# Optimization experiments

Measured on AMD Instinct MI355X. Metric: run time of the kernel, lower is better.

Reference implementation:

```python
import jax, jax.numpy as jnp
import numpy as np

N, E, E_LG, H, KGE, NUM_GRAPHS, N_ITER = 100000, 500000, 1000000, 128, 128, 1024, 2
EPS = 1e-5

def _prelu(x, a):
    return jnp.where(x >= 0, x, a * x)

def _seg_mean(vals, idx, num):
    s = jax.ops.segment_sum(vals, idx, num_segments=num)
    c = jax.ops.segment_sum(jnp.ones((vals.shape[0],), vals.dtype), idx, num_segments=num)
    return s / jnp.maximum(c, 1.0)[:, None]

def setup_inputs() -> dict:
    key = jax.random.key(0)
    ks = jax.random.split(key, 16)
    sc = 1.0 / np.sqrt(H)
    inp = {
        "x": jax.random.normal(ks[0], (N, H), jnp.float32),
        "edge_attr": jax.random.normal(ks[1], (E, H), jnp.float32),
        "edge_index": jax.random.randint(ks[2], (2, E), 0, N),
        "batch": jnp.sort(jax.random.randint(ks[3], (N,), 0, NUM_GRAPHS)),
        "line_graph_edge_index": jax.random.randint(ks[4], (2, E_LG), 0, E),
        # edge_update_net: Linear + PReLU + BatchNorm1d (eval mode)
        "W1": jax.random.normal(ks[5], (H, H), jnp.float32) * sc,
        "b1": jnp.zeros((H,), jnp.float32),
        "a1": jnp.full((1,), 0.25, jnp.float32),
        "bn_gamma": jnp.ones((H,), jnp.float32),
        "bn_beta": jnp.zeros((H,), jnp.float32),
        "bn_mean": jnp.zeros((H,), jnp.float32),
        "bn_var": jnp.ones((H,), jnp.float32),
        # GRU (single layer, single step)
        "w_ih": jax.random.normal(ks[6], (3 * H, H), jnp.float32) * sc,
        "w_hh": jax.random.normal(ks[7], (3 * H, H), jnp.float32) * sc,
        "b_ih": jnp.zeros((3 * H,), jnp.float32),
        "b_hh": jnp.zeros((3 * H,), jnp.float32),
        # DynamicAttention net
        "Wa1": jax.random.normal(ks[8], (H // 2, H), jnp.float32) * sc,
        "ba1": jnp.zeros((H // 2,), jnp.float32),
        "a2": jnp.full((1,), 0.25, jnp.float32),
        "Wa2": jax.random.normal(ks[9], (1, H // 2), jnp.float32) * (1.0 / np.sqrt(H // 2)),
        "ba2": jnp.zeros((1,), jnp.float32),
        # readout
        "Wr": jax.random.normal(ks[10], (KGE, H), jnp.float32) * sc,
        "br": jnp.zeros((KGE,), jnp.float32),
    }
    return inp

def reference(x, edge_attr, W1, b1, a1, bn_gamma, bn_beta, bn_mean, bn_var,
              w_ih, w_hh, b_ih, b_hh, Wa1, ba1, a2, Wa2, ba2, Wr, br,
              edge_index, batch, line_graph_edge_index):
    src, dst = edge_index[0], edge_index[1]
    l_src, l_dst = line_graph_edge_index[0], line_graph_edge_index[1]
    h = x  # GRU hidden state [N, H]
    for _ in range(N_ITER):
        # edge-to-edge message passing (node_to_edge_proj is Identity here)
        fused = edge_attr + (x[src] + x[dst]) * 0.5  # [E, H]
        agg = _seg_mean(fused[l_src], l_dst, E)      # scatter-mean over line graph
        upd = _prelu(agg @ W1.T + b1, a1)
        upd = (upd - bn_mean) * jax.lax.rsqrt(bn_var + EPS) * bn_gamma + bn_beta
        fused = fused + upd
        node_updates = _seg_mean(fused, dst, N)      # [N, H]
        # single GRU step
        gi = node_updates @ w_ih.T + b_ih
        gh = h @ w_hh.T + b_hh
        gi_r, gi_z, gi_n = jnp.split(gi, 3, axis=-1)
        gh_r, gh_z, gh_n = jnp.split(gh, 3, axis=-1)
        r = jax.nn.sigmoid(gi_r + gh_r)
        z = jax.nn.sigmoid(gi_z + gh_z)
        n = jnp.tanh(gi_n + r * gh_n)
        h = (1.0 - z) * n + z * h
        x = h
    # dynamic attention: per-graph scalar gate
    graph_repr = _seg_mean(x, batch, NUM_GRAPHS)     # [G, H]
    attn = jax.nn.sigmoid(_prelu(graph_repr @ Wa1.T + ba1, a2) @ Wa2.T + ba2)  # [G, 1]
    attended = x * attn[batch]
    graph_emb = jax.ops.segment_sum(attended, batch, num_segments=NUM_GRAPHS)
    graph_emb = graph_emb @ Wr.T + br
    return (x, graph_emb)
```

## Files before the change

kernel.cpp:

```cpp
#include <hip/hip_runtime.h>
#include <stdint.h>

#define H 128
#define G_NUM 1024
#define BN_EPS 1e-5f

typedef unsigned int uint;
typedef unsigned short ushort;
typedef __attribute__((ext_vector_type(8))) __bf16 bf16x8;
typedef __attribute__((ext_vector_type(8))) ushort ushort8;
typedef __attribute__((ext_vector_type(4))) float f32x4;

__device__ __forceinline__ float b2f(ushort u){ return __uint_as_float(((uint)u) << 16); }
__device__ __forceinline__ ushort f2b(float f){
    uint u = __float_as_uint(f);
    u += 0x7FFFu + ((u >> 16) & 1u);
    return (ushort)(u >> 16);
}
__device__ __forceinline__ float ldf(const void* p, size_t i, int bf){
    return bf ? b2f(((const ushort*)p)[i]) : ((const float*)p)[i];
}
__device__ __forceinline__ int swz(int r, int byte_in_row){
    return (r * 256 + byte_in_row) ^ ((r & 7) << 4);
}

__global__ void k_probe(const uint* __restrict__ gamma_bits, int* __restrict__ flag){
    if (threadIdx.x == 0 && blockIdx.x == 0)
        *flag = (gamma_bits[0] == 0x3F803F80u) ? 1 : 0;
}

__global__ __launch_bounds__(256) void k_count_i(const int* __restrict__ idx, int* __restrict__ cnt, int n){
    int t = blockIdx.x * 256 + threadIdx.x;
    if (t < n) atomicAdd(&cnt[idx[t]], 1);
}
__global__ __launch_bounds__(256) void k_scan_reduce(const int* __restrict__ cnt, int* __restrict__ bsum, int n){
    int base = blockIdx.x * 1024;
    int s = 0;
    for (int i = threadIdx.x; i < 1024; i += 256){ int idx = base + i; s += (idx < n) ? cnt[idx] : 0; }
    __shared__ int r[256];
    r[threadIdx.x] = s; __syncthreads();
    for (int o = 128; o > 0; o >>= 1){ if (threadIdx.x < o) r[threadIdx.x] += r[threadIdx.x + o]; __syncthreads(); }
    if (threadIdx.x == 0) bsum[blockIdx.x] = r[0];
}
__global__ void k_scan_bsum(int* __restrict__ bsum, int nb){
    if (threadIdx.x == 0 && blockIdx.x == 0){
        int acc = 0;
        for (int i = 0; i < nb; i++){ int v = bsum[i]; bsum[i] = acc; acc += v; }
    }
}
__global__ __launch_bounds__(256) void k_scan_final(const int* __restrict__ cnt, const int* __restrict__ bsum,
                                                    int* __restrict__ off, int n){
    __shared__ int ts[256];
    int base = blockIdx.x * 1024;
    int tid = threadIdx.x;
    int loc[4]; int s = 0;
    #pragma unroll
    for (int j = 0; j < 4; j++){
        int idx = base + tid * 4 + j;
        loc[j] = s;
        s += (idx < n) ? cnt[idx] : 0;
    }
    ts[tid] = s; __syncthreads();
    for (int o = 1; o < 256; o <<= 1){
        int v = (tid >= o) ? ts[tid - o] : 0;
        __syncthreads();
        ts[tid] += v;
        __syncthreads();
    }
    int texcl = ts[tid] - s + bsum[blockIdx.x];
    #pragma unroll
    for (int j = 0; j < 4; j++){
        int idx = base + tid * 4 + j;
        if (idx < n) off[idx] = texcl + loc[j];
    }
}
__global__ void k_sent(int* __restrict__ lg_off, int E, int ELG, int* __restrict__ nd_off, int N, int Etot){
    if (threadIdx.x == 0){ lg_off[E] = ELG; nd_off[N] = Etot; }
}
__global__ void k_zero2(ushort* __restrict__ a, ushort* __restrict__ b, size_t off){
    int t = threadIdx.x;
    a[off + t] = 0; b[off + t] = 0;
}
__global__ __launch_bounds__(256) void k_fill(const int* __restrict__ keys, const int* __restrict__ vals,
                                              const int* __restrict__ off, int* __restrict__ cur,
                                              int* __restrict__ list, int n){
    int t = blockIdx.x * 256 + threadIdx.x;
    if (t >= n) return;
    int k = keys[t];
    int pos = atomicAdd(&cur[k], 1);
    list[off[k] + pos] = vals ? vals[t] : t;
}
__global__ __launch_bounds__(256) void k_cvt(const void* __restrict__ in, float* __restrict__ out,
                                             int n, const int* __restrict__ flag){
    int t = blockIdx.x * 256 + threadIdx.x;
    if (t < n) out[t] = ldf(in, t, *flag);
}
__global__ __launch_bounds__(256) void k_cvt_bf(const void* __restrict__ in, ushort* __restrict__ out,
                                                int n, const int* __restrict__ flag){
    int t = blockIdx.x * 256 + threadIdx.x;
    if (t >= n) return;
    if (*flag) out[t] = ((const ushort*)in)[t];
    else       out[t] = f2b(((const float*)in)[t]);
}
__global__ __launch_bounds__(256) void k_transpose(const void* __restrict__ in, float* __restrict__ out,
                                                   int R, int C, const int* __restrict__ flag){
    int t = blockIdx.x * 256 + threadIdx.x;
    if (t >= R * C) return;
    int bf = *flag;
    int r = t / C, c = t - r * C;
    out[c * R + r] = ldf(in, t, bf);
}
__global__ void k_ep(const void* b1, const void* a1, const void* gam, const void* bet,
                     const void* mean, const void* var, float* __restrict__ ep, const int* __restrict__ flag){
    int c = threadIdx.x; int bf = *flag;
    ep[c]       = ldf(b1, c, bf);
    ep[128 + c] = rsqrtf(ldf(var, c, bf) + BN_EPS) * ldf(gam, c, bf);
    ep[256 + c] = ldf(mean, c, bf);
    ep[384 + c] = ldf(bet, c, bf);
    if (c == 0) ep[512] = ldf(a1, 0, bf);
}
__global__ __launch_bounds__(256) void k_store_h(const ushort* __restrict__ hb, void* __restrict__ out,
                                                 int n, const int* __restrict__ flag){
    int t = blockIdx.x * 256 + threadIdx.x;
    if (t >= n) return;
    ushort v = hb[t];
    if (*flag) ((ushort*)out)[t] = v;
    else       ((float*) out)[t] = b2f(v);
}

__global__ __launch_bounds__(256) void k_fused(const void* __restrict__ ea, const ushort* __restrict__ hb,
                                               const int* __restrict__ ei, ushort* __restrict__ fused,
                                               int E, const int* __restrict__ flag){
    int t = blockIdx.x * 256 + threadIdx.x;
    if (t >= E * 32) return;
    int bf = *flag;
    int e = t >> 5, c = (t & 31) * 4;
    int s = ei[e], d = ei[E + e];
    ushort4 hs = *(const ushort4*)(hb + (size_t)s * H + c);
    ushort4 hd = *(const ushort4*)(hb + (size_t)d * H + c);
    size_t base = (size_t)e * H + c;
    float a0, a1, a2, a3;
    if (bf){
        ushort4 av = *(const ushort4*)((const ushort*)ea + base);
        a0 = b2f(av.x); a1 = b2f(av.y); a2 = b2f(av.z); a3 = b2f(av.w);
    } else {
        float4 av = *(const float4*)((const float*)ea + base);
        a0 = av.x; a1 = av.y; a2 = av.z; a3 = av.w;
    }
    ushort4 o;
    o.x = f2b(a0 + 0.5f * (b2f(hs.x) + b2f(hd.x)));
    o.y = f2b(a1 + 0.5f * (b2f(hs.y) + b2f(hd.y)));
    o.z = f2b(a2 + 0.5f * (b2f(hs.z) + b2f(hd.z)));
    o.w = f2b(a3 + 0.5f * (b2f(hs.w) + b2f(hd.w)));
    *(ushort4*)(fused + base) = o;
}


__global__ __launch_bounds__(256) void k_agg_gemm(const ushort* __restrict__ fused,
                                                  const int* __restrict__ lg_off, const int* __restrict__ lg_list,
                                                  const ushort* __restrict__ W1bf, const float* __restrict__ ep,
                                                  ushort* __restrict__ fused2, int E, int LMAX){
    __shared__ __attribute__((aligned(16))) char As[32 * 256];
    __shared__ int offL[33];
    int tid = threadIdx.x, wid = tid >> 6, lane = tid & 63;
    int r0 = blockIdx.x * 32;
    if (tid < 33) offL[tid] = lg_off[r0 + tid];
    __syncthreads();
    int l16 = lane >> 4, ch16 = lane & 15;
    int rA = wid * 8 + l16, rB = rA + 4;
    int baseA = offL[rA], degA = offL[rA + 1] - baseA;
    int baseB = offL[rB], degB = offL[rB + 1] - baseB;
    int dm = max(degA, degB);
    #pragma unroll
    for (int o = 32; o > 0; o >>= 1) dm = max(dm, __shfl_xor(dm, o));
    float accA[8] = {}, accB[8] = {};
    #pragma unroll 2
    for (int i = 0; i < dm; i++){
        int liA = baseA + i; liA = (liA < LMAX) ? liA : (LMAX - 1);
        int liB = baseB + i; liB = (liB < LMAX) ? liB : (LMAX - 1);
        int sA = lg_list[liA];
        int sB = lg_list[liB];
        sA = (i < degA) ? sA : E;
        sB = (i < degB) ? sB : E;
        ushort8 vA = *(const ushort8*)(fused + (size_t)sA * H + ch16 * 8);
        ushort8 vB = *(const ushort8*)(fused + (size_t)sB * H + ch16 * 8);
        #pragma unroll
        for (int j = 0; j < 8; j++){ accA[j] += b2f(vA[j]); accB[j] += b2f(vB[j]); }
    }
    float invA = 1.f / fmaxf((float)degA, 1.f);
    float invB = 1.f / fmaxf((float)degB, 1.f);
    ushort8 oA, oB;
    #pragma unroll
    for (int j = 0; j < 8; j++){ oA[j] = f2b(accA[j] * invA); oB[j] = f2b(accB[j] * invB); }
    *(ushort8*)(As + swz(rA, ch16 * 16)) = oA;
    *(ushort8*)(As + swz(rB, ch16 * 16)) = oB;
    __syncthreads();
    int lrow = lane & 15, lhi = lane >> 4;
    f32x4 acc[2][2] = {};
    #pragma unroll
    for (int ks = 0; ks < 4; ks++){
        bf16x8 afr[2];
        #pragma unroll
        for (int rt = 0; rt < 2; rt++)
            afr[rt] = *(const bf16x8*)(As + swz(rt * 16 + lrow, ks * 64 + lhi * 16));
        #pragma unroll
        for (int cc = 0; cc < 2; cc++){
            int c = (2 * wid + cc) * 16 + lrow;
            bf16x8 bfr = *(const bf16x8*)(W1bf + (size_t)c * H + ks * 32 + lhi * 8);
            #pragma unroll
            for (int rt = 0; rt < 2; rt++)
                acc[cc][rt] = __builtin_amdgcn_mfma_f32_16x16x32_bf16(afr[rt], bfr, acc[cc][rt], 0, 0, 0);
        }
    }
    float aa = ep[512];
    #pragma unroll
    for (int cc = 0; cc < 2; cc++){
        int c = (2 * wid + cc) * 16 + lrow;
        float bb = ep[c], sc = ep[128 + c], mb = ep[256 + c], be = ep[384 + c];
        #pragma unroll
        for (int rt = 0; rt < 2; rt++)
            #pragma unroll
            for (int rg = 0; rg < 4; rg++){
                int r = rt * 16 + lhi * 4 + rg;
                float u = acc[cc][rt][rg] + bb;
                u = (u >= 0.f) ? u : aa * u;
                u = (u - mb) * sc + be;
                size_t idx = (size_t)(r0 + r) * H + c;
                fused2[idx] = f2b(b2f(fused[idx]) + u);
            }
    }
}

__global__ __launch_bounds__(256) void k_gru(const ushort* __restrict__ fused2,
                                             const int* __restrict__ nd_off, const int* __restrict__ nd_list,
                                             ushort* __restrict__ hb,
                                             const ushort* __restrict__ wihbf, const ushort* __restrict__ whhbf,
                                             const float* __restrict__ bi, const float* __restrict__ bh,
                                             int N, int EZ, int LMAX){
    __shared__ __attribute__((aligned(16))) char NUs[32 * 256];
    __shared__ __attribute__((aligned(16))) char HHs[32 * 256];
    __shared__ int offL[33];
    int tid = threadIdx.x, wid = tid >> 6, lane = tid & 63;
    int r0 = blockIdx.x * 32;
    if (tid < 33) offL[tid] = nd_off[r0 + tid];
    int l16 = lane >> 4, ch16 = lane & 15;
    int rA = wid * 8 + l16, rB = rA + 4;
    *(ushort8*)(HHs + swz(rA, ch16 * 16)) = *(const ushort8*)(hb + (size_t)(r0 + rA) * H + ch16 * 8);
    *(ushort8*)(HHs + swz(rB, ch16 * 16)) = *(const ushort8*)(hb + (size_t)(r0 + rB) * H + ch16 * 8);
    __syncthreads();
    int baseA = offL[rA], degA = offL[rA + 1] - baseA;
    int baseB = offL[rB], degB = offL[rB + 1] - baseB;
    int dm = max(degA, degB);
    #pragma unroll
    for (int o = 32; o > 0; o >>= 1) dm = max(dm, __shfl_xor(dm, o));
    float accA[8] = {}, accB[8] = {};
    #pragma unroll 2
    for (int i = 0; i < dm; i++){
        int liA = baseA + i; liA = (liA < LMAX) ? liA : (LMAX - 1);
        int liB = baseB + i; liB = (liB < LMAX) ? liB : (LMAX - 1);
        int sA = nd_list[liA];
        int sB = nd_list[liB];
        sA = (i < degA) ? sA : EZ;
        sB = (i < degB) ? sB : EZ;
        ushort8 vA = *(const ushort8*)(fused2 + (size_t)sA * H + ch16 * 8);
        ushort8 vB = *(const ushort8*)(fused2 + (size_t)sB * H + ch16 * 8);
        #pragma unroll
        for (int j = 0; j < 8; j++){ accA[j] += b2f(vA[j]); accB[j] += b2f(vB[j]); }
    }
    float invA = 1.f / fmaxf((float)degA, 1.f);
    float invB = 1.f / fmaxf((float)degB, 1.f);
    ushort8 oA, oB;
    #pragma unroll
    for (int j = 0; j < 8; j++){ oA[j] = f2b(accA[j] * invA); oB[j] = f2b(accB[j] * invB); }
    *(ushort8*)(NUs + swz(rA, ch16 * 16)) = oA;
    *(ushort8*)(NUs + swz(rB, ch16 * 16)) = oB;
    __syncthreads();
    int lrow = lane & 15, lhi = lane >> 4;
    #pragma unroll
    for (int b = 0; b < 2; b++){
        f32x4 aI[3][2] = {}, aH[3][2] = {};
        #pragma unroll
        for (int ks = 0; ks < 4; ks++){
            bf16x8 fN[2], fH[2];
            #pragma unroll
            for (int rt = 0; rt < 2; rt++){
                int addr = swz(rt * 16 + lrow, ks * 64 + lhi * 16);
                fN[rt] = *(const bf16x8*)(NUs + addr);
                fH[rt] = *(const bf16x8*)(HHs + addr);
            }
            #pragma unroll
            for (int g = 0; g < 3; g++){
                int c = g * 128 + (wid + 4 * b) * 16 + lrow;
                bf16x8 bI = *(const bf16x8*)(wihbf + (size_t)c * H + ks * 32 + lhi * 8);
                bf16x8 bH = *(const bf16x8*)(whhbf + (size_t)c * H + ks * 32 + lhi * 8);
                #pragma unroll
                for (int rt = 0; rt < 2; rt++){
                    aI[g][rt] = __builtin_amdgcn_mfma_f32_16x16x32_bf16(fN[rt], bI, aI[g][rt], 0, 0, 0);
                    aH[g][rt] = __builtin_amdgcn_mfma_f32_16x16x32_bf16(fH[rt], bH, aH[g][rt], 0, 0, 0);
                }
            }
        }
        int c = (wid + 4 * b) * 16 + lrow;
        float bir = bi[c], biz = bi[128 + c], bin = bi[256 + c];
        float bhr = bh[c], bhz = bh[128 + c], bhn = bh[256 + c];
        #pragma unroll
        for (int rt = 0; rt < 2; rt++)
            #pragma unroll
            for (int rg = 0; rg < 4; rg++){
                int r = rt * 16 + lhi * 4 + rg;
                int n = r0 + r;
                float gr = aI[0][rt][rg] + bir + aH[0][rt][rg] + bhr;
                float gz = aI[1][rt][rg] + biz + aH[1][rt][rg] + bhz;
                float rv = 1.f / (1.f + __expf(-gr));
                float zv = 1.f / (1.f + __expf(-gz));
                float nv = tanhf(aI[2][rt][rg] + bin + rv * (aH[2][rt][rg] + bhn));
                float hold = b2f(*(const ushort*)(HHs + swz(r, c * 2)));
                hb[(size_t)n * H + c] = f2b((1.f - zv) * nv + zv * hold);
            }
    }
}

__global__ __launch_bounds__(256) void k_gbounds(const int* __restrict__ batch, int* __restrict__ gs, int N, int G){
    int g = blockIdx.x * 256 + threadIdx.x;
    if (g > G) return;
    int lo = 0, hi = N;
    while (lo < hi){ int mid = (lo + hi) >> 1; if (batch[mid] < g) lo = mid + 1; else hi = mid; }
    gs[g] = lo;
}
__global__ __launch_bounds__(256) void k_graph_sum(const ushort* __restrict__ hb, const int* __restrict__ gs,
                                                   float* __restrict__ gsum){
    int g = blockIdx.x, c = threadIdx.x & 127, half = threadIdx.x >> 7;
    int s = gs[g], e = gs[g + 1];
    float acc0 = 0.f, acc1 = 0.f;
    int r = s + half;
    for (; r + 2 < e; r += 4){
        acc0 += b2f(hb[(size_t)r * H + c]);
        acc1 += b2f(hb[(size_t)(r + 2) * H + c]);
    }
    for (; r < e; r += 2) acc0 += b2f(hb[(size_t)r * H + c]);
    __shared__ float tmp[128];
    if (half == 1) tmp[c] = acc0 + acc1;
    __syncthreads();
    if (half == 0) gsum[(size_t)g * H + c] = acc0 + acc1 + tmp[c];
}
__global__ void k_attn(const float* __restrict__ gsum, const int* __restrict__ gs,
                       const void* __restrict__ Wa1, const void* __restrict__ ba1,
                       const void* __restrict__ a2, const void* __restrict__ Wa2,
                       const void* __restrict__ ba2, float* __restrict__ attn, const int* __restrict__ flag){
    int g = blockIdx.x;
    int j = threadIdx.x;
    int bf = *flag;
    float inv = 1.0f / fmaxf((float)(gs[g + 1] - gs[g]), 1.0f);
    __shared__ float R[H];
    for (int i = j; i < H; i += 64) R[i] = gsum[(size_t)g * H + i] * inv;
    __syncthreads();
    float t = 0.f;
    for (int k = 0; k < H; k++) t += R[k] * ldf(Wa1, (size_t)j * H + k, bf);
    t += ldf(ba1, j, bf);
    float al = ldf(a2, 0, bf);
    t = (t >= 0.f) ? t : al * t;
    float p = t * ldf(Wa2, j, bf);
    #pragma unroll
    for (int o = 32; o > 0; o >>= 1) p += __shfl_down(p, o);
    if (j == 0) attn[g] = 1.f / (1.f + __expf(-(p + ldf(ba2, 0, bf))));
}
__global__ __launch_bounds__(256) void k_graph_gemm(const float* __restrict__ gsum, const float* __restrict__ attn,
                                                    const float* __restrict__ WrT,
                                                    const void* __restrict__ br, void* __restrict__ out,
                                                    size_t obase, const int* __restrict__ flag){
    __shared__ float A[8 * H];
    int bf = *flag;
    int r0 = blockIdx.x * 8;
    for (int i = threadIdx.x; i < 8 * H; i += 256){
        int r = i >> 7;
        A[i] = gsum[(size_t)(r0 + r) * H + (i & 127)] * attn[r0 + r];
    }
    __syncthreads();
    int c = threadIdx.x & 127;
    int rr = (threadIdx.x >> 7) * 4;
    float acc[4] = {0, 0, 0, 0};
    for (int k = 0; k < H; k++){
        float w = WrT[k * H + c];
        #pragma unroll
        for (int j = 0; j < 4; j++) acc[j] += A[(rr + j) * H + k] * w;
    }
    float bb = ldf(br, c, bf);
    for (int j = 0; j < 4; j++){
        size_t idx = obase + (size_t)(r0 + rr + j) * H + c;
        float v = acc[j] + bb;
        if (bf) ((ushort*)out)[idx] = f2b(v);
        else    ((float*) out)[idx] = v;
    }
}

extern "C" void kernel_launch(void* const* d_in, const int* in_sizes, int n_in,
                              void* d_out, int out_size, void* d_ws, size_t ws_size,
                              hipStream_t stream)
{
    const void* x    = d_in[0];
    const void* ea   = d_in[1];
    const int*  ei   = (const int*)d_in[2];
    const int*  batch= (const int*)d_in[3];
    const int*  lgi  = (const int*)d_in[4];
    const void* W1   = d_in[5];
    const void* b1   = d_in[6];
    const void* a1   = d_in[7];
    const void* bng  = d_in[8];
    const void* bnb  = d_in[9];
    const void* bnm  = d_in[10];
    const void* bnv  = d_in[11];
    const void* wih  = d_in[12];
    const void* whh  = d_in[13];
    const void* bih  = d_in[14];
    const void* bhh  = d_in[15];
    const void* Wa1  = d_in[16];
    const void* ba1  = d_in[17];
    const void* a2   = d_in[18];
    const void* Wa2  = d_in[19];
    const void* ba2  = d_in[20];
    const void* Wr   = d_in[21];
    const void* br   = d_in[22];

    const int N   = in_sizes[0] / H;
    const int E   = in_sizes[1] / H;
    const int ELG = in_sizes[4] / 2;
    const int G   = G_NUM;
    const int nb_lg = (E + 1023) / 1024;
    const int nb_nd = (N + 1023) / 1024;

    char* ws = (char*)d_ws;
    size_t off = 0;
    auto alloc = [&](size_t b) -> void* { void* p = ws + off; off += (b + 255) & ~(size_t)255; return p; };
    int*    flag   = (int*)   alloc(256);
    ushort* hb     = (ushort*)alloc((size_t)N * H * 2);
    ushort* fused  = (ushort*)alloc((size_t)(E + 1) * H * 2);
    ushort* fused2 = (ushort*)alloc((size_t)(E + 1) * H * 2);
    int*    zreg   = (int*)   alloc((size_t)(2 * E + 2 * N) * 4);
    int*    lg_cnt = zreg;
    int*    nd_cnt = zreg + E;
    int*    lg_cur = zreg + E + N;
    int*    nd_cur = zreg + 2 * E + N;
    int*    lg_off = (int*)   alloc((size_t)(E + 1) * 4);
    int*    nd_off = (int*)   alloc((size_t)(N + 1) * 4);
    int*    lg_list= (int*)   alloc((size_t)ELG * 4);
    int*    nd_list= (int*)   alloc((size_t)E * 4);
    int*    bsumA  = (int*)   alloc((size_t)(nb_lg + 8) * 4);
    int*    bsumB  = (int*)   alloc((size_t)(nb_nd + 8) * 4);
    int*    gs     = (int*)   alloc((size_t)(G + 1) * 4);
    ushort* W1bf   = (ushort*)alloc(128 * 128 * 2);
    ushort* wihbf  = (ushort*)alloc(384 * 128 * 2);
    ushort* whhbf  = (ushort*)alloc(384 * 128 * 2);
    float*  ep     = (float*) alloc(513 * 4);
    float*  bi     = (float*) alloc(384 * 4);
    float*  bh     = (float*) alloc(384 * 4);
    float*  WrT    = (float*) alloc(128 * 128 * 4);
    float*  gsum   = (float*) alloc((size_t)G * H * 4);
    float*  attn   = (float*) alloc((size_t)G * 4);

    k_probe<<<1, 64, 0, stream>>>((const uint*)bng, flag);

    hipMemsetAsync(zreg, 0, (size_t)(2 * E + 2 * N) * 4, stream);
    k_count_i<<<(ELG + 255) / 256, 256, 0, stream>>>(lgi + ELG, lg_cnt, ELG);
    k_count_i<<<(E + 255) / 256, 256, 0, stream>>>(ei + E, nd_cnt, E);
    k_scan_reduce<<<nb_lg, 256, 0, stream>>>(lg_cnt, bsumA, E);
    k_scan_bsum<<<1, 64, 0, stream>>>(bsumA, nb_lg);
    k_scan_final<<<nb_lg, 256, 0, stream>>>(lg_cnt, bsumA, lg_off, E);
    k_scan_reduce<<<nb_nd, 256, 0, stream>>>(nd_cnt, bsumB, N);
    k_scan_bsum<<<1, 64, 0, stream>>>(bsumB, nb_nd);
    k_scan_final<<<nb_nd, 256, 0, stream>>>(nd_cnt, bsumB, nd_off, N);
    k_sent<<<1, 64, 0, stream>>>(lg_off, E, ELG, nd_off, N, E);
    k_fill<<<(ELG + 255) / 256, 256, 0, stream>>>(lgi + ELG, lgi, lg_off, lg_cur, lg_list, ELG);
    k_fill<<<(E + 255) / 256, 256, 0, stream>>>(ei + E, (const int*)nullptr, nd_off, nd_cur, nd_list, E);
    k_zero2<<<1, 128, 0, stream>>>(fused, fused2, (size_t)E * H);

    k_cvt_bf<<<(128 * 128 + 255) / 256, 256, 0, stream>>>(W1, W1bf, 128 * 128, flag);
    k_cvt_bf<<<(384 * 128 + 255) / 256, 256, 0, stream>>>(wih, wihbf, 384 * 128, flag);
    k_cvt_bf<<<(384 * 128 + 255) / 256, 256, 0, stream>>>(whh, whhbf, 384 * 128, flag);
    k_ep<<<1, 128, 0, stream>>>(b1, a1, bng, bnb, bnm, bnv, ep, flag);
    k_cvt<<<(384 + 255) / 256, 256, 0, stream>>>(bih, bi, 384, flag);
    k_cvt<<<(384 + 255) / 256, 256, 0, stream>>>(bhh, bh, 384, flag);
    k_transpose<<<(128 * 128 + 255) / 256, 256, 0, stream>>>(Wr, WrT, 128, 128, flag);

    k_cvt_bf<<<(N * H + 255) / 256, 256, 0, stream>>>(x, hb, N * H, flag);

    for (int it = 0; it < 2; it++){
        k_fused<<<(E * 32 + 255) / 256, 256, 0, stream>>>(ea, hb, ei, fused, E, flag);
        k_agg_gemm<<<(E + 31) / 32, 256, 0, stream>>>(fused, lg_off, lg_list, W1bf, ep, fused2, E, ELG);
        k_gru<<<(N + 31) / 32, 256, 0, stream>>>(fused2, nd_off, nd_list, hb, wihbf, whhbf, bi, bh, N, E, E);
    }

    k_gbounds<<<(G + 256) / 256, 256, 0, stream>>>(batch, gs, N, G);
    k_graph_sum<<<G, 256, 0, stream>>>(hb, gs, gsum);
    k_attn<<<G, 64, 0, stream>>>(gsum, gs, Wa1, ba1, a2, Wa2, ba2, attn, flag);
    k_graph_gemm<<<G / 8, 256, 0, stream>>>(gsum, attn, WrT, br, d_out, (size_t)N * H, flag);
    k_store_h<<<(N * H + 255) / 256, 256, 0, stream>>>(hb, d_out, N * H, flag);
}
```

Measured before the change: 1.062 ms.

## Merge CSR build kernels, widen vector loads, stage epilogue stores through LDS

Merges the line-graph and node CSR construction into one concatenated count/scan/fill pipeline and replaces the serial block-sum scan with a parallel one. Several small parameter-conversion launches are folded into fewer kernels. The fused kernel now uses 8-wide vector loads and stores. The agg_gemm and GRU epilogues write results to LDS and then store whole coalesced rows, instead of issuing scattered 2-byte global writes. The wave-wide max-degree shuffle is removed and the gather loop unroll is raised. Together these aim to cut launch overhead and uncoalesced stores, at the cost of extra LDS traffic and syncs.

```diff
diff --git a/kernel.cpp b/kernel.cpp
--- a/kernel.cpp
+++ b/kernel.cpp
@@ -29,9 +29,11 @@
         *flag = (gamma_bits[0] == 0x3F803F80u) ? 1 : 0;
 }
 
-__global__ __launch_bounds__(256) void k_count_i(const int* __restrict__ idx, int* __restrict__ cnt, int n){
-    int t = blockIdx.x * 256 + threadIdx.x;
-    if (t < n) atomicAdd(&cnt[idx[t]], 1);
+__global__ __launch_bounds__(256) void k_count2(const int* __restrict__ lgi, const int* __restrict__ ei,
+                                                int* __restrict__ cnt, int ELG, int E){
+    int t = blockIdx.x * 256 + threadIdx.x;
+    if (t < ELG) atomicAdd(&cnt[lgi[ELG + t]], 1);
+    else { int t2 = t - ELG; if (t2 < E) atomicAdd(&cnt[E + ei[E + t2]], 1); }
 }
 __global__ __launch_bounds__(256) void k_scan_reduce(const int* __restrict__ cnt, int* __restrict__ bsum, int n){
     int base = blockIdx.x * 1024;
@@ -42,10 +44,28 @@
     for (int o = 128; o > 0; o >>= 1){ if (threadIdx.x < o) r[threadIdx.x] += r[threadIdx.x + o]; __syncthreads(); }
     if (threadIdx.x == 0) bsum[blockIdx.x] = r[0];
 }
-__global__ void k_scan_bsum(int* __restrict__ bsum, int nb){
-    if (threadIdx.x == 0 && blockIdx.x == 0){
-        int acc = 0;
-        for (int i = 0; i < nb; i++){ int v = bsum[i]; bsum[i] = acc; acc += v; }
+__global__ __launch_bounds__(256) void k_scan_mid(int* __restrict__ bsum, int nb){
+    __shared__ int ts[256];
+    int tid = threadIdx.x;
+    int loc[4]; int s = 0;
+    #pragma unroll
+    for (int j = 0; j < 4; j++){
+        int idx = tid * 4 + j;
+        loc[j] = s;
+        s += (idx < nb) ? bsum[idx] : 0;
+    }
+    ts[tid] = s; __syncthreads();
+    for (int o = 1; o < 256; o <<= 1){
+        int v = (tid >= o) ? ts[tid - o] : 0;
+        __syncthreads();
+        ts[tid] += v;
+        __syncthreads();
+    }
+    int texcl = ts[tid] - s;
+    #pragma unroll
+    for (int j = 0; j < 4; j++){
+        int idx = tid * 4 + j;
+        if (idx < nb) bsum[idx] = texcl + loc[j];
     }
 }
 __global__ __launch_bounds__(256) void k_scan_final(const int* __restrict__ cnt, const int* __restrict__ bsum,
@@ -74,33 +94,46 @@
         if (idx < n) off[idx] = texcl + loc[j];
     }
 }
-__global__ void k_sent(int* __restrict__ lg_off, int E, int ELG, int* __restrict__ nd_off, int N, int Etot){
-    if (threadIdx.x == 0){ lg_off[E] = ELG; nd_off[N] = Etot; }
+__global__ void k_sent1(int* __restrict__ off, int idx, int val){
+    if (threadIdx.x == 0) off[idx] = val;
+}
+__global__ __launch_bounds__(256) void k_fill2(const int* __restrict__ lgi, const int* __restrict__ ei,
+                                               const int* __restrict__ off, int* __restrict__ cur,
+                                               int* __restrict__ list, int ELG, int E){
+    int t = blockIdx.x * 256 + threadIdx.x;
+    if (t < ELG){
+        int k = lgi[ELG + t];
+        int pos = atomicAdd(&cur[k], 1);
+        list[off[k] + pos] = lgi[t];
+    } else {
+        int t2 = t - ELG;
+        if (t2 < E){
+            int k = E + ei[E + t2];
+            int pos = atomicAdd(&cur[k], 1);
+            list[off[k] + pos] = t2;
+        }
+    }
 }
 __global__ void k_zero2(ushort* __restrict__ a, ushort* __restrict__ b, size_t off){
     int t = threadIdx.x;
     a[off + t] = 0; b[off + t] = 0;
 }
-__global__ __launch_bounds__(256) void k_fill(const int* __restrict__ keys, const int* __restrict__ vals,
-                                              const int* __restrict__ off, int* __restrict__ cur,
-                                              int* __restrict__ list, int n){
-    int t = blockIdx.x * 256 + threadIdx.x;
-    if (t >= n) return;
-    int k = keys[t];
-    int pos = atomicAdd(&cur[k], 1);
-    list[off[k] + pos] = vals ? vals[t] : t;
-}
-__global__ __launch_bounds__(256) void k_cvt(const void* __restrict__ in, float* __restrict__ out,
-                                             int n, const int* __restrict__ flag){
-    int t = blockIdx.x * 256 + threadIdx.x;
-    if (t < n) out[t] = ldf(in, t, *flag);
-}
 __global__ __launch_bounds__(256) void k_cvt_bf(const void* __restrict__ in, ushort* __restrict__ out,
                                                 int n, const int* __restrict__ flag){
     int t = blockIdx.x * 256 + threadIdx.x;
     if (t >= n) return;
     if (*flag) out[t] = ((const ushort*)in)[t];
     else       out[t] = f2b(((const float*)in)[t]);
+}
+__global__ __launch_bounds__(256) void k_wcvt(const void* __restrict__ W1, const void* __restrict__ wih,
+                                              const void* __restrict__ whh,
+                                              ushort* __restrict__ W1bf, ushort* __restrict__ wihbf,
+                                              ushort* __restrict__ whhbf, const int* __restrict__ flag){
+    int t = blockIdx.x * 256 + threadIdx.x;
+    int bf = *flag;
+    if (t < 16384) W1bf[t] = bf ? ((const ushort*)W1)[t] : f2b(((const float*)W1)[t]);
+    else if (t < 65536){ int i = t - 16384; wihbf[i] = bf ? ((const ushort*)wih)[i] : f2b(((const float*)wih)[i]); }
+    else if (t < 114688){ int i = t - 65536; whhbf[i] = bf ? ((const ushort*)whh)[i] : f2b(((const float*)whh)[i]); }
 }
 __global__ __launch_bounds__(256) void k_transpose(const void* __restrict__ in, float* __restrict__ out,
                                                    int R, int C, const int* __restrict__ flag){
@@ -110,14 +143,20 @@
     int r = t / C, c = t - r * C;
     out[c * R + r] = ldf(in, t, bf);
 }
-__global__ void k_ep(const void* b1, const void* a1, const void* gam, const void* bet,
-                     const void* mean, const void* var, float* __restrict__ ep, const int* __restrict__ flag){
-    int c = threadIdx.x; int bf = *flag;
-    ep[c]       = ldf(b1, c, bf);
-    ep[128 + c] = rsqrtf(ldf(var, c, bf) + BN_EPS) * ldf(gam, c, bf);
-    ep[256 + c] = ldf(mean, c, bf);
-    ep[384 + c] = ldf(bet, c, bf);
-    if (c == 0) ep[512] = ldf(a1, 0, bf);
+__global__ void k_params(const void* b1, const void* a1, const void* gam, const void* bet,
+                         const void* mean, const void* var, const void* bih, const void* bhh,
+                         float* __restrict__ ep, float* __restrict__ bi, float* __restrict__ bh,
+                         const int* __restrict__ flag){
+    int t = threadIdx.x; int bf = *flag;
+    bi[t] = ldf(bih, t, bf);
+    bh[t] = ldf(bhh, t, bf);
+    if (t < 128){
+        ep[t]       = ldf(b1, t, bf);
+        ep[128 + t] = rsqrtf(ldf(var, t, bf) + BN_EPS) * ldf(gam, t, bf);
+        ep[256 + t] = ldf(mean, t, bf);
+        ep[384 + t] = ldf(bet, t, bf);
+    }
+    if (t == 0) ep[512] = ldf(a1, 0, bf);
 }
 __global__ __launch_bounds__(256) void k_store_h(const ushort* __restrict__ hb, void* __restrict__ out,
                                                  int n, const int* __restrict__ flag){
@@ -132,54 +171,52 @@
                                                const int* __restrict__ ei, ushort* __restrict__ fused,
                                                int E, const int* __restrict__ flag){
     int t = blockIdx.x * 256 + threadIdx.x;
-    if (t >= E * 32) return;
+    if (t >= E * 16) return;
     int bf = *flag;
-    int e = t >> 5, c = (t & 31) * 4;
+    int e = t >> 4, ch = (t & 15) * 8;
     int s = ei[e], d = ei[E + e];
-    ushort4 hs = *(const ushort4*)(hb + (size_t)s * H + c);
-    ushort4 hd = *(const ushort4*)(hb + (size_t)d * H + c);
-    size_t base = (size_t)e * H + c;
-    float a0, a1, a2, a3;
+    ushort8 hs = *(const ushort8*)(hb + (size_t)s * H + ch);
+    ushort8 hd = *(const ushort8*)(hb + (size_t)d * H + ch);
+    size_t base = (size_t)e * H + ch;
+    float av[8];
     if (bf){
-        ushort4 av = *(const ushort4*)((const ushort*)ea + base);
-        a0 = b2f(av.x); a1 = b2f(av.y); a2 = b2f(av.z); a3 = b2f(av.w);
+        ushort8 a = *(const ushort8*)((const ushort*)ea + base);
+        #pragma unroll
+        for (int j = 0; j < 8; j++) av[j] = b2f(a[j]);
     } else {
-        float4 av = *(const float4*)((const float*)ea + base);
-        a0 = av.x; a1 = av.y; a2 = av.z; a3 = av.w;
-    }
-    ushort4 o;
-    o.x = f2b(a0 + 0.5f * (b2f(hs.x) + b2f(hd.x)));
-    o.y = f2b(a1 + 0.5f * (b2f(hs.y) + b2f(hd.y)));
-    o.z = f2b(a2 + 0.5f * (b2f(hs.z) + b2f(hd.z)));
-    o.w = f2b(a3 + 0.5f * (b2f(hs.w) + b2f(hd.w)));
-    *(ushort4*)(fused + base) = o;
-}
-
+        float4 a0 = *(const float4*)((const float*)ea + base);
+        float4 a1 = *(const float4*)((const float*)ea + base + 4);
+        av[0] = a0.x; av[1] = a0.y; av[2] = a0.z; av[3] = a0.w;
+        av[4] = a1.x; av[5] = a1.y; av[6] = a1.z; av[7] = a1.w;
+    }
+    ushort8 o;
+    #pragma unroll
+    for (int j = 0; j < 8; j++) o[j] = f2b(av[j] + 0.5f * (b2f(hs[j]) + b2f(hd[j])));
+    *(ushort8*)(fused + base) = o;
+}
 
 __global__ __launch_bounds__(256) void k_agg_gemm(const ushort* __restrict__ fused,
-                                                  const int* __restrict__ lg_off, const int* __restrict__ lg_list,
+                                                  const int* __restrict__ off_cat, const int* __restrict__ list,
                                                   const ushort* __restrict__ W1bf, const float* __restrict__ ep,
                                                   ushort* __restrict__ fused2, int E, int LMAX){
     __shared__ __attribute__((aligned(16))) char As[32 * 256];
     __shared__ int offL[33];
     int tid = threadIdx.x, wid = tid >> 6, lane = tid & 63;
     int r0 = blockIdx.x * 32;
-    if (tid < 33) offL[tid] = lg_off[r0 + tid];
+    if (tid < 33) offL[tid] = off_cat[r0 + tid];
     __syncthreads();
     int l16 = lane >> 4, ch16 = lane & 15;
     int rA = wid * 8 + l16, rB = rA + 4;
     int baseA = offL[rA], degA = offL[rA + 1] - baseA;
     int baseB = offL[rB], degB = offL[rB + 1] - baseB;
     int dm = max(degA, degB);
-    #pragma unroll
-    for (int o = 32; o > 0; o >>= 1) dm = max(dm, __shfl_xor(dm, o));
     float accA[8] = {}, accB[8] = {};
-    #pragma unroll 2
+    #pragma unroll 4
     for (int i = 0; i < dm; i++){
         int liA = baseA + i; liA = (liA < LMAX) ? liA : (LMAX - 1);
         int liB = baseB + i; liB = (liB < LMAX) ? liB : (LMAX - 1);
-        int sA = lg_list[liA];
-        int sB = lg_list[liB];
+        int sA = list[liA];
+        int sB = list[liB];
         sA = (i < degA) ? sA : E;
         sB = (i < degB) ? sB : E;
         ushort8 vA = *(const ushort8*)(fused + (size_t)sA * H + ch16 * 8);
@@ -212,6 +249,7 @@
                 acc[cc][rt] = __builtin_amdgcn_mfma_f32_16x16x32_bf16(afr[rt], bfr, acc[cc][rt], 0, 0, 0);
         }
     }
+    __syncthreads();
     float aa = ep[512];
     #pragma unroll
     for (int cc = 0; cc < 2; cc++){
@@ -225,14 +263,25 @@
                 float u = acc[cc][rt][rg] + bb;
                 u = (u >= 0.f) ? u : aa * u;
                 u = (u - mb) * sc + be;
-                size_t idx = (size_t)(r0 + r) * H + c;
-                fused2[idx] = f2b(b2f(fused[idx]) + u);
+                *(ushort*)(As + swz(r, c * 2)) = f2b(u);
             }
     }
+    __syncthreads();
+    #pragma unroll
+    for (int q = 0; q < 2; q++){
+        int r = (q == 0) ? rA : rB;
+        size_t gbase = (size_t)(r0 + r) * H + ch16 * 8;
+        ushort8 f = *(const ushort8*)(fused + gbase);
+        ushort8 u = *(const ushort8*)(As + swz(r, ch16 * 16));
+        ushort8 o;
+        #pragma unroll
+        for (int j = 0; j < 8; j++) o[j] = f2b(b2f(f[j]) + b2f(u[j]));
+        *(ushort8*)(fused2 + gbase) = o;
+    }
 }
 
 __global__ __launch_bounds__(256) void k_gru(const ushort* __restrict__ fused2,
-                                             const int* __restrict__ nd_off, const int* __restrict__ nd_list,
+                                             const int* __restrict__ off_cat, const int* __restrict__ list,
                                              ushort* __restrict__ hb,
                                              const ushort* __restrict__ wihbf, const ushort* __restrict__ whhbf,
                                              const float* __restrict__ bi, const float* __restrict__ bh,
@@ -242,7 +291,7 @@
     __shared__ int offL[33];
     int tid = threadIdx.x, wid = tid >> 6, lane = tid & 63;
     int r0 = blockIdx.x * 32;
-    if (tid < 33) offL[tid] = nd_off[r0 + tid];
+    if (tid < 33) offL[tid] = off_cat[r0 + tid];
     int l16 = lane >> 4, ch16 = lane & 15;
     int rA = wid * 8 + l16, rB = rA + 4;
     *(ushort8*)(HHs + swz(rA, ch16 * 16)) = *(const ushort8*)(hb + (size_t)(r0 + rA) * H + ch16 * 8);
@@ -251,15 +300,13 @@
     int baseA = offL[rA], degA = offL[rA + 1] - baseA;
     int baseB = offL[rB], degB = offL[rB + 1] - baseB;
     int dm = max(degA, degB);
-    #pragma unroll
-    for (int o = 32; o > 0; o >>= 1) dm = max(dm, __shfl_xor(dm, o));
     float accA[8] = {}, accB[8] = {};
-    #pragma unroll 2
+    #pragma unroll 4
     for (int i = 0; i < dm; i++){
         int liA = baseA + i; liA = (liA < LMAX) ? liA : (LMAX - 1);
         int liB = baseB + i; liB = (liB < LMAX) ? liB : (LMAX - 1);
-        int sA = nd_list[liA];
-        int sB = nd_list[liB];
+        int sA = list[liA];
+        int sB = list[liB];
         sA = (i < degA) ? sA : EZ;
         sB = (i < degB) ? sB : EZ;
         ushort8 vA = *(const ushort8*)(fused2 + (size_t)sA * H + ch16 * 8);
@@ -276,6 +323,7 @@
     *(ushort8*)(NUs + swz(rB, ch16 * 16)) = oB;
     __syncthreads();
     int lrow = lane & 15, lhi = lane >> 4;
+    ushort hnew[2][2][4];
     #pragma unroll
     for (int b = 0; b < 2; b++){
         f32x4 aI[3][2] = {}, aH[3][2] = {};
@@ -308,16 +356,30 @@
             #pragma unroll
             for (int rg = 0; rg < 4; rg++){
                 int r = rt * 16 + lhi * 4 + rg;
-                int n = r0 + r;
                 float gr = aI[0][rt][rg] + bir + aH[0][rt][rg] + bhr;
                 float gz = aI[1][rt][rg] + biz + aH[1][rt][rg] + bhz;
                 float rv = 1.f / (1.f + __expf(-gr));
                 float zv = 1.f / (1.f + __expf(-gz));
                 float nv = tanhf(aI[2][rt][rg] + bin + rv * (aH[2][rt][rg] + bhn));
                 float hold = b2f(*(const ushort*)(HHs + swz(r, c * 2)));
-                hb[(size_t)n * H + c] = f2b((1.f - zv) * nv + zv * hold);
+                hnew[b][rt][rg] = f2b((1.f - zv) * nv + zv * hold);
             }
     }
+    __syncthreads();
+    #pragma unroll
+    for (int b = 0; b < 2; b++){
+        int c = (wid + 4 * b) * 16 + lrow;
+        #pragma unroll
+        for (int rt = 0; rt < 2; rt++)
+            #pragma unroll
+            for (int rg = 0; rg < 4; rg++){
+                int r = rt * 16 + lhi * 4 + rg;
+                *(ushort*)(NUs + swz(r, c * 2)) = hnew[b][rt][rg];
+            }
+    }
+    __syncthreads();
+    *(ushort8*)(hb + (size_t)(r0 + rA) * H + ch16 * 8) = *(const ushort8*)(NUs + swz(rA, ch16 * 16));
+    *(ushort8*)(hb + (size_t)(r0 + rB) * H + ch16 * 8) = *(const ushort8*)(NUs + swz(rB, ch16 * 16));
 }
 
 __global__ __launch_bounds__(256) void k_gbounds(const int* __restrict__ batch, int* __restrict__ gs, int N, int G){
@@ -425,68 +487,54 @@
     const int E   = in_sizes[1] / H;
     const int ELG = in_sizes[4] / 2;
     const int G   = G_NUM;
-    const int nb_lg = (E + 1023) / 1024;
-    const int nb_nd = (N + 1023) / 1024;
+    const int NK  = E + N;
+    const int nb  = (NK + 1023) / 1024;
 
     char* ws = (char*)d_ws;
     size_t off = 0;
     auto alloc = [&](size_t b) -> void* { void* p = ws + off; off += (b + 255) & ~(size_t)255; return p; };
-    int*    flag   = (int*)   alloc(256);
-    ushort* hb     = (ushort*)alloc((size_t)N * H * 2);
-    ushort* fused  = (ushort*)alloc((size_t)(E + 1) * H * 2);
-    ushort* fused2 = (ushort*)alloc((size_t)(E + 1) * H * 2);
-    int*    zreg   = (int*)   alloc((size_t)(2 * E + 2 * N) * 4);
-    int*    lg_cnt = zreg;
-    int*    nd_cnt = zreg + E;
-    int*    lg_cur = zreg + E + N;
-    int*    nd_cur = zreg + 2 * E + N;
-    int*    lg_off = (int*)   alloc((size_t)(E + 1) * 4);
-    int*    nd_off = (int*)   alloc((size_t)(N + 1) * 4);
-    int*    lg_list= (int*)   alloc((size_t)ELG * 4);
-    int*    nd_list= (int*)   alloc((size_t)E * 4);
-    int*    bsumA  = (int*)   alloc((size_t)(nb_lg + 8) * 4);
-    int*    bsumB  = (int*)   alloc((size_t)(nb_nd + 8) * 4);
-    int*    gs     = (int*)   alloc((size_t)(G + 1) * 4);
-    ushort* W1bf   = (ushort*)alloc(128 * 128 * 2);
-    ushort* wihbf  = (ushort*)alloc(384 * 128 * 2);
-    ushort* whhbf  = (ushort*)alloc(384 * 128 * 2);
-    float*  ep     = (float*) alloc(513 * 4);
-    float*  bi     = (float*) alloc(384 * 4);
-    float*  bh     = (float*) alloc(384 * 4);
-    float*  WrT    = (float*) alloc(128 * 128 * 4);
-    float*  gsum   = (float*) alloc((size_t)G * H * 4);
-    float*  attn   = (float*) alloc((size_t)G * 4);
+    int*    flag    = (int*)   alloc(256);
+    ushort* hb      = (ushort*)alloc((size_t)N * H * 2);
+    ushort* fused   = (ushort*)alloc((size_t)(E + 1) * H * 2);
+    ushort* fused2  = (ushort*)alloc((size_t)(E + 1) * H * 2);
+    int*    zreg    = (int*)   alloc((size_t)(2 * NK) * 4);
+    int*    cnt_cat = zreg;
+    int*    cur_cat = zreg + NK;
+    int*    off_cat = (int*)   alloc((size_t)(NK + 1) * 4);
+    int*    list_cat= (int*)   alloc((size_t)(ELG + E) * 4);
+    int*    bsum    = (int*)   alloc((size_t)(nb + 8) * 4);
+    int*    gs      = (int*)   alloc((size_t)(G + 1) * 4);
+    ushort* W1bf    = (ushort*)alloc(128 * 128 * 2);
+    ushort* wihbf   = (ushort*)alloc(384 * 128 * 2);
+    ushort* whhbf   = (ushort*)alloc(384 * 128 * 2);
+    float*  ep      = (float*) alloc(513 * 4);
+    float*  bi      = (float*) alloc(384 * 4);
+    float*  bh      = (float*) alloc(384 * 4);
+    float*  WrT     = (float*) alloc(128 * 128 * 4);
+    float*  gsum    = (float*) alloc((size_t)G * H * 4);
+    float*  attn    = (float*) alloc((size_t)G * 4);
 
     k_probe<<<1, 64, 0, stream>>>((const uint*)bng, flag);
 
-    hipMemsetAsync(zreg, 0, (size_t)(2 * E + 2 * N) * 4, stream);
-    k_count_i<<<(ELG + 255) / 256, 256, 0, stream>>>(lgi + ELG, lg_cnt, ELG);
-    k_count_i<<<(E + 255) / 256, 256, 0, stream>>>(ei + E, nd_cnt, E);
-    k_scan_reduce<<<nb_lg, 256, 0, stream>>>(lg_cnt, bsumA, E);
-    k_scan_bsum<<<1, 64, 0, stream>>>(bsumA, nb_lg);
-    k_scan_final<<<nb_lg, 256, 0, stream>>>(lg_cnt, bsumA, lg_off, E);
-    k_scan_reduce<<<nb_nd, 256, 0, stream>>>(nd_cnt, bsumB, N);
-    k_scan_bsum<<<1, 64, 0, stream>>>(bsumB, nb_nd);
-    k_scan_final<<<nb_nd, 256, 0, stream>>>(nd_cnt, bsumB, nd_off, N);
-    k_sent<<<1, 64, 0, stream>>>(lg_off, E, ELG, nd_off, N, E);
-    k_fill<<<(ELG + 255) / 256, 256, 0, stream>>>(lgi + ELG, lgi, lg_off, lg_cur, lg_list, ELG);
-    k_fill<<<(E + 255) / 256, 256, 0, stream>>>(ei + E, (const int*)nullptr, nd_off, nd_cur, nd_list, E);
+    hipMemsetAsync(zreg, 0, (size_t)(2 * NK) * 4, stream);
+    k_count2<<<(ELG + E + 255) / 256, 256, 0, stream>>>(lgi, ei, cnt_cat, ELG, E);
+    k_scan_reduce<<<nb, 256, 0, stream>>>(cnt_cat, bsum, NK);
+    k_scan_mid<<<1, 256, 0, stream>>>(bsum, nb);
+    k_scan_final<<<nb, 256, 0, stream>>>(cnt_cat, bsum, off_cat, NK);
+    k_sent1<<<1, 64, 0, stream>>>(off_cat, NK, ELG + E);
+    k_fill2<<<(ELG + E + 255) / 256, 256, 0, stream>>>(lgi, ei, off_cat, cur_cat, list_cat, ELG, E);
     k_zero2<<<1, 128, 0, stream>>>(fused, fused2, (size_t)E * H);
 
-    k_cvt_bf<<<(128 * 128 + 255) / 256, 256, 0, stream>>>(W1, W1bf, 128 * 128, flag);
-    k_cvt_bf<<<(384 * 128 + 255) / 256, 256, 0, stream>>>(wih, wihbf, 384 * 128, flag);
-    k_cvt_bf<<<(384 * 128 + 255) / 256, 256, 0, stream>>>(whh, whhbf, 384 * 128, flag);
-    k_ep<<<1, 128, 0, stream>>>(b1, a1, bng, bnb, bnm, bnv, ep, flag);
-    k_cvt<<<(384 + 255) / 256, 256, 0, stream>>>(bih, bi, 384, flag);
-    k_cvt<<<(384 + 255) / 256, 256, 0, stream>>>(bhh, bh, 384, flag);
+    k_wcvt<<<(114688 + 255) / 256, 256, 0, stream>>>(W1, wih, whh, W1bf, wihbf, whhbf, flag);
+    k_params<<<1, 384, 0, stream>>>(b1, a1, bng, bnb, bnm, bnv, bih, bhh, ep, bi, bh, flag);
     k_transpose<<<(128 * 128 + 255) / 256, 256, 0, stream>>>(Wr, WrT, 128, 128, flag);
 
     k_cvt_bf<<<(N * H + 255) / 256, 256, 0, stream>>>(x, hb, N * H, flag);
 
     for (int it = 0; it < 2; it++){
-        k_fused<<<(E * 32 + 255) / 256, 256, 0, stream>>>(ea, hb, ei, fused, E, flag);
-        k_agg_gemm<<<(E + 31) / 32, 256, 0, stream>>>(fused, lg_off, lg_list, W1bf, ep, fused2, E, ELG);
-        k_gru<<<(N + 31) / 32, 256, 0, stream>>>(fused2, nd_off, nd_list, hb, wihbf, whhbf, bi, bh, N, E, E);
+        k_fused<<<(E * 16 + 255) / 256, 256, 0, stream>>>(ea, hb, ei, fused, E, flag);
+        k_agg_gemm<<<(E + 31) / 32, 256, 0, stream>>>(fused, off_cat, list_cat, W1bf, ep, fused2, E, ELG);
+        k_gru<<<(N + 31) / 32, 256, 0, stream>>>(fused2, off_cat + E, list_cat, hb, wihbf, whhbf, bi, bh, N, E, ELG + E);
     }
 
     k_gbounds<<<(G + 256) / 256, 256, 0, stream>>>(batch, gs, N, G);
```

Result: faster. 1.012 ms (-4.7%).
